# Performance work log

Measured on AMD Instinct MI355X. Metric: run time of the kernel, lower is better.

The kernel has to match this reference:

```python
import jax, jax.numpy as jnp
import numpy as np

A, H, DK, DM = 13, 16, 4, 256   # num_attention, n_head, d_k, d_model
DH = DM // H                    # per-head value dim = 16
MLP_OUT = 128
EPS = 1e-5
TEMP = float(np.sqrt(DK))
IN_CH = 10


def setup_inputs() -> dict:
    key = jax.random.key(0)
    ks = jax.random.split(key, 12)
    B, T = 1024, 60
    x = jax.random.normal(ks[0], (B, T, IN_CH), dtype=jnp.float32)
    # inconv (1x1 Conv1d == Linear over channels)
    Wc = jax.random.normal(ks[1], (DM, IN_CH), dtype=jnp.float32) * 0.1
    bc = jax.random.normal(ks[2], (DM,), dtype=jnp.float32) * 0.01
    # in_norm GroupNorm affine
    gn_in_w = jnp.ones((DM,), jnp.float32)
    gn_in_b = jnp.zeros((DM,), jnp.float32)
    # learned query + key projection (std = sqrt(2/d_k) per torch init)
    Q = jax.random.normal(ks[3], (A, H, DK), dtype=jnp.float32) * float(np.sqrt(2.0 / DK))
    Wk = jax.random.normal(ks[4], (A * H * DK, DM), dtype=jnp.float32) * float(np.sqrt(2.0 / DK))
    bk = jnp.zeros((A * H * DK,), jnp.float32)
    # MLP: Linear(256,128) + BatchNorm1d(128) (eval mode) + ReLU
    W1 = jax.random.normal(ks[5], (MLP_OUT, DM), dtype=jnp.float32) * 0.05
    b1 = jnp.zeros((MLP_OUT,), jnp.float32)
    bn_w = jnp.ones((MLP_OUT,), jnp.float32)
    bn_b = jnp.zeros((MLP_OUT,), jnp.float32)
    bn_rm = jnp.zeros((MLP_OUT,), jnp.float32)
    bn_rv = jnp.ones((MLP_OUT,), jnp.float32)
    # out_norm GroupNorm affine
    gn_out_w = jnp.ones((MLP_OUT,), jnp.float32)
    gn_out_b = jnp.zeros((MLP_OUT,), jnp.float32)
    return dict(x=x, Wc=Wc, bc=bc, gn_in_w=gn_in_w, gn_in_b=gn_in_b, Q=Q,
                Wk=Wk, bk=bk, W1=W1, b1=b1, bn_w=bn_w, bn_b=bn_b,
                bn_rm=bn_rm, bn_rv=bn_rv, gn_out_w=gn_out_w, gn_out_b=gn_out_b)


def _ltae_fwd(x, Wc, bc, gn_in_w, gn_in_b, Q, Wk, bk, W1, b1,
              bn_w, bn_b, bn_rm, bn_rv, gn_out_w, gn_out_b):
    B, T, _ = x.shape
    # inconv: 1x1 conv over channel dim
    h = jnp.einsum('btc,dc->btd', x, Wc) + bc                      # [B,T,DM]
    # in_norm: GroupNorm(H groups) over [B, DM, T] -> normalize per (sample, group) over (C/G, T)
    g = h.transpose(0, 2, 1).reshape(B, H, DM // H, T)
    mu = g.mean(axis=(2, 3), keepdims=True)
    var = g.var(axis=(2, 3), keepdims=True)
    g = (g - mu) / jnp.sqrt(var + EPS)
    v = (g.reshape(B, DM, T) * gn_in_w[None, :, None] + gn_in_b[None, :, None]).transpose(0, 2, 1)
    # ---- MultiHeadAttention (faithful to original reshape/view ordering) ----
    # q: stack Q along batch dim 2 then flatten -> row order (a, h, b)
    q = jnp.broadcast_to(Q[:, :, None, :], (A, H, B, DK)).reshape(-1, DK)      # [A*H*B, DK]
    # k: Linear then permute(3,0,1,2,4).view(-1,T,DK) (reproduces torch's contiguous flatten)
    k = (jnp.einsum('btd,ed->bte', v, Wk) + bk).reshape(B, T, A, H, DK)
    k = k.transpose(3, 0, 1, 2, 4).reshape(-1, T, DK)                          # [H*B*A, T, DK]
    # v heads: stack(split) -> [H, B, T, DH] -> [H*B, T, DH]
    vh = v.reshape(B, T, H, DH).transpose(2, 0, 1, 3).reshape(H * B, T, DH)
    attn = jnp.einsum('nd,ntd->nt', q, k) / TEMP                               # [N, T]
    attn = jax.nn.softmax(attn, axis=-1)                                       # dropout = identity (eval)
    ve = jnp.broadcast_to(vh[:, None], (H * B, A, T, DH)).reshape(-1, T, DH)   # [H*B*A, T, DH]
    out = jnp.einsum('nt,ntd->nd', attn, ve)                                   # [N, DH]
    out = out.reshape(A, H, B, DH)
    # ---- head concat + MLP ----
    out = out.transpose(0, 2, 1, 3).reshape(A * B, DM)
    y = out @ W1.T + b1
    y = (y - bn_rm) / jnp.sqrt(bn_rv + EPS) * bn_w + bn_b                      # BatchNorm1d eval
    y = jax.nn.relu(y)                                                          # dropout = identity (eval)
    # out_norm: GroupNorm(H, MLP_OUT) on 2D input: per-sample per-group norm
    g = y.reshape(A * B, H, MLP_OUT // H)
    mu = g.mean(axis=2, keepdims=True)
    var = g.var(axis=2, keepdims=True)
    y = ((g - mu) / jnp.sqrt(var + EPS)).reshape(A * B, MLP_OUT) * gn_out_w + gn_out_b
    return y.reshape(A, B, MLP_OUT).transpose(1, 0, 2)                          # [B, A, MLP_OUT]


def reference(x, Wc, bc, gn_in_w, gn_in_b, Q, Wk, bk, W1, b1,
              bn_w, bn_b, bn_rm, bn_rv, gn_out_w, gn_out_b):
    return _ltae_fwd(x, Wc, bc, gn_in_w, gn_in_b, Q, Wk, bk, W1, b1,
                     bn_w, bn_b, bn_rm, bn_rv, gn_out_w, gn_out_b)
```

## Files before the change

kernel.cpp:

```cpp
#include <hip/hip_runtime.h>
#include <hip/hip_bf16.h>
#include <math.h>

#define NB   1024
#define NT   60
#define NC   10
#define NDM  256
#define NH   16
#define NDH  16
#define NA   13
#define NM   208
#define NMO  128

#define WROW6 4096

#define OFF_WEFF  0
#define N_WEFF    (NH*14*WROW6)
#define OFF_BEFF  (OFF_WEFF + N_WEFF)
#define N_BEFF    (NM*NH*NA)
#define OFF_VGT   (OFF_BEFF + N_BEFF)
#define N_VGT     (NB*NDM*64)
#define OFF_ATT   (OFF_VGT + N_VGT)
#define N_ATT     (NM*NB*NDH)

#define LDS_FENCE() __asm__ __volatile__("s_waitcnt lgkmcnt(0)" ::: "memory")

__global__ void ltae_weff(const float* __restrict__ Q, const float* __restrict__ Wk,
                          const float* __restrict__ bk, float* __restrict__ weff6,
                          float* __restrict__ beff2) {
    int blk = blockIdx.x;
    int hk = blk / 14, mi = blk - hk*14;
    int m  = hk*13 + mi;
    int mc = m > 207 ? 207 : m;
    int d = threadIdx.x;
    float q0 = Q[mc*4+0], q1 = Q[mc*4+1], q2 = Q[mc*4+2], q3 = Q[mc*4+3];
    int g = d >> 1, dl = d & 1;
    size_t base = (size_t)blk*WROW6 + g*32 + dl*13;
#pragma unroll
    for (int ak = 0; ak < NA; ++ak) {
        int e = (ak*16 + hk)*4;
        float w = q0*Wk[(size_t)(e+0)*NDM + d] + q1*Wk[(size_t)(e+1)*NDM + d]
                + q2*Wk[(size_t)(e+2)*NDM + d] + q3*Wk[(size_t)(e+3)*NDM + d];
        weff6[base + ak] = w;
    }
    if (dl == 1) {
#pragma unroll
        for (int p = 26; p < 32; ++p) weff6[(size_t)blk*WROW6 + g*32 + p] = 0.f;
    }
    if (d < NA && m <= 207) {
        int e = (d*16 + hk)*4;
        beff2[(m*16 + hk)*NA + d] = q0*bk[e] + q1*bk[e+1] + q2*bk[e+2] + q3*bk[e+3];
    }
}

#define VT_S 66
#define K1_LDS_BYTES ((NDM*VT_S + NT*NC)*4)

__launch_bounds__(1024, 8)
__global__ void ltae_convgn(const float* __restrict__ x, const float* __restrict__ Wc,
                            const float* __restrict__ bc, const float* __restrict__ gnw,
                            const float* __restrict__ gnb, float* __restrict__ vgT) {
    extern __shared__ float smem[];
    float* Vt = smem;
    float* xs = smem + NDM*VT_S;
    int b = blockIdx.x, tid = threadIdx.x;
    if (tid < NT*NC) xs[tid] = x[(size_t)b*NT*NC + tid];
    __syncthreads();
    {
        int d = tid >> 2, q = tid & 3;
        float wc[NC];
#pragma unroll
        for (int c = 0; c < NC; ++c) wc[c] = Wc[d*NC + c];
        float bcv = bc[d];
        float h[15];
        float s1 = 0.f, s2 = 0.f;
#pragma unroll
        for (int k = 0; k < 15; ++k) {
            int t = 15*q + k;
            float a = bcv;
#pragma unroll
            for (int c = 0; c < NC; ++c) a = fmaf(xs[t*NC + c], wc[c], a);
            h[k] = a; s1 += a; s2 += a*a;
        }
#pragma unroll
        for (int off = 1; off < 64; off <<= 1) {
            s1 += __shfl_xor(s1, off);
            s2 += __shfl_xor(s2, off);
        }
        float mean = s1 * (1.f/960.f);
        float var  = s2 * (1.f/960.f) - mean*mean;
        float rstd = rsqrtf(var + 1e-5f);
        float g = gnw[d], bb = gnb[d];
#pragma unroll
        for (int k = 0; k < 15; ++k)
            Vt[d*VT_S + 15*q + k] = (h[k]-mean)*rstd*g + bb;
    }
    __syncthreads();
    float* vb = vgT + (size_t)b*NDM*64;
    for (int i = tid; i < NDM*16; i += 1024) {
        int d = i >> 4, t4 = (i & 15) << 2;
        float4 o;
        o.x = (t4+0 < NT) ? Vt[d*VT_S + t4+0] : 0.f;
        o.y = (t4+1 < NT) ? Vt[d*VT_S + t4+1] : 0.f;
        o.z = (t4+2 < NT) ? Vt[d*VT_S + t4+2] : 0.f;
        o.w = (t4+3 < NT) ? Vt[d*VT_S + t4+3] : 0.f;
        *(float4*)&vb[d*64 + t4] = o;
    }
}

#define BSTRIDE (NDM*64)
__launch_bounds__(128, 8)
__global__ void ltae_attn(const float* __restrict__ vgT, const float* __restrict__ weff6,
                          const float* __restrict__ beff2, float* __restrict__ attout) {
    __shared__ float wbuf[2*784];
    int p = blockIdx.x;
    int xcd = p & 7, idx = p >> 3;
    int b   = xcd * 128 + (idx >> 3);
    int hkp = idx & 7;
    int tid = threadIdx.x;
    int wid = tid >> 6, lane = tid & 63;
    int hk = __builtin_amdgcn_readfirstlane(hkp*2 + wid);
    int tk = lane;
    int mi0   = (13*b) >> 10;
    int rstar = ((mi0+1) << 10) - 13*b;
    const float* __restrict__ wrow = weff6 + (size_t)(hk*14 + mi0)*WROW6;
    const float* __restrict__ vX   = vgT + (size_t)b*BSTRIDE + tk;
    float* myC = wbuf + wid*784;

    float acc[13];
#pragma unroll
    for (int j = 0; j < 13; ++j) acc[j] = 0.f;

#pragma unroll 1
    for (int gg = 0; gg < 64; ++gg) {
        const float* wgA = wrow + (size_t)(2*gg)*32;
        const float* wgB = wrow + (size_t)(2*gg+1)*32;
        float a0 = vX[(4*gg+0)*64];
        float a1 = vX[(4*gg+1)*64];
        float c0 = vX[(4*gg+2)*64];
        float c1 = vX[(4*gg+3)*64];
#pragma unroll
        for (int ak = 0; ak < 13; ++ak)
            acc[ak] = fmaf(a1, wgA[13+ak], fmaf(a0, wgA[ak], acc[ak]));
#pragma unroll
        for (int ak = 0; ak < 13; ++ak)
            acc[ak] = fmaf(c1, wgB[13+ak], fmaf(c0, wgB[ak], acc[ak]));
    }

    if (rstar < 13) {
        int ustar = 60*rstar;
        int tstar = (ustar >= 1) ? (ustar/13) : -1;
        if (tk == tstar) {
#pragma unroll
            for (int j = 0; j < 13; ++j) myC[j] = acc[j];
        }
        LDS_FENCE();
        if (tk >= tstar) {
#pragma unroll
            for (int j = 0; j < 13; ++j) acc[j] = 0.f;
            const float* __restrict__ wrow2 = weff6 + (size_t)(hk*14 + mi0 + 1)*WROW6;
#pragma unroll 1
            for (int g = 0; g < 128; ++g) {
                const float* wg = wrow2 + g*32;
                float v0 = vX[(2*g)*64];
                float v1 = vX[(2*g+1)*64];
#pragma unroll
                for (int ak = 0; ak < 13; ++ak)
                    acc[ak] = fmaf(v1, wg[13+ak], fmaf(v0, wg[ak], acc[ak]));
            }
        }
        if (tk == tstar) {
#pragma unroll
            for (int j = 0; j < 13; ++j)
                if (13*tk + j < ustar) acc[j] = myC[j];
        }
        LDS_FENCE();
    }

    int dh = lane >> 2, cc = lane & 3;
    int hb13 = (hk*1024 + b)*13;
    if (tk < NT) {
#pragma unroll
        for (int j = 0; j < 13; ++j) myC[13*tk + j] = acc[j];
    }
    LDS_FENCE();
    float vreg[15];
#pragma unroll
    for (int j = 0; j < 15; ++j)
        vreg[j] = vgT[((size_t)b*NDM + hk*16 + dh)*64 + cc + 4*j];
#pragma unroll 1
    for (int r = 0; r < 13; ++r) {
        int n = hb13 + r;
        int m = n >> 10;
        int brow = (m*16 + hk)*13;
        float logit = -1e30f;
        if (lane < NT) {
            int u  = r*60 + lane;
            int ak = u % 13;
            logit = (myC[u] + beff2[brow + ak]) * 0.5f;
        }
        float mx = logit;
#pragma unroll
        for (int off = 32; off; off >>= 1) mx = fmaxf(mx, __shfl_xor(mx, off));
        float e = (lane < NT) ? __expf(logit - mx) : 0.f;
        float s = e;
#pragma unroll
        for (int off = 32; off; off >>= 1) s += __shfl_xor(s, off);
        float attn = e / s;
        if (lane < NT) myC[r*60 + lane] = attn;
        LDS_FENCE();
        float a = 0.f;
#pragma unroll
        for (int j = 0; j < 15; ++j)
            a = fmaf(myC[r*60 + cc + 4*j], vreg[j], a);
        a += __shfl_xor(a, 1);
        a += __shfl_xor(a, 2);
        if (cc == 0) attout[(size_t)n*NDH + dh] = a;
    }
}

#define FS 260
__launch_bounds__(1024)
__global__ void ltae_mlp(const float* __restrict__ attout, const float* __restrict__ W1,
                         const float* __restrict__ b1, const float* __restrict__ bnw,
                         const float* __restrict__ bnb, const float* __restrict__ bnrm,
                         const float* __restrict__ bnrv, const float* __restrict__ gow,
                         const float* __restrict__ gob, float* __restrict__ out) {
    __shared__ float f[16*FS];
    int tid = threadIdx.x;
    int sl  = tid & 7;
    int j   = tid >> 3;
    int base = blockIdx.x << 4;
    for (int k = tid; k < 16*NDM; k += 1024) {
        int s = k >> 8, c = k & 255;
        int sid2 = base + s;
        int aa = sid2 >> 10, bb = sid2 & 1023;
        int h2 = c >> 4, dhh = c & 15;
        f[s*FS + c] = attout[((size_t)((aa*16 + h2)*1024 + bb))*NDH + dhh];
    }
    __syncthreads();
    const float* fr0 = f + sl*FS;
    const float* fr1 = f + (sl+8)*FS;
    const float* w   = &W1[(size_t)j*NDM];
    float bj = b1[j];
    float acc0 = bj, acc1 = bj;
    for (int c = 0; c < NDM; c += 4) {
        float4 wv = *(const float4*)&w[c];
        float4 f0 = *(const float4*)&fr0[c];
        float4 f1 = *(const float4*)&fr1[c];
        acc0 += wv.x*f0.x + wv.y*f0.y + wv.z*f0.z + wv.w*f0.w;
        acc1 += wv.x*f1.x + wv.y*f1.y + wv.z*f1.z + wv.w*f1.w;
    }
    float rs = rsqrtf(bnrv[j] + 1e-5f);
    float sc = rs * bnw[j];
    float sh = bnb[j] - bnrm[j]*sc;
    float y0 = fmaxf(acc0*sc + sh, 0.f);
    float y1 = fmaxf(acc1*sc + sh, 0.f);
    float a1 = y0, b1s = y0*y0, a2 = y1, b2s = y1*y1;
#pragma unroll
    for (int off = 8; off < 64; off <<= 1) {
        a1  += __shfl_xor(a1, off);
        b1s += __shfl_xor(b1s, off);
        a2  += __shfl_xor(a2, off);
        b2s += __shfl_xor(b2s, off);
    }
    float gw = gow[j], gb = gob[j];
    {
        float mean = a1 * 0.125f;
        float var  = b1s * 0.125f - mean*mean;
        float o = (y0 - mean) * rsqrtf(var + 1e-5f) * gw + gb;
        int sid = base + sl, aa = sid >> 10, bb = sid & 1023;
        out[((size_t)bb*NA + aa)*NMO + j] = o;
    }
    {
        float mean = a2 * 0.125f;
        float var  = b2s * 0.125f - mean*mean;
        float o = (y1 - mean) * rsqrtf(var + 1e-5f) * gw + gb;
        int sid = base + sl + 8, aa = sid >> 10, bb = sid & 1023;
        out[((size_t)bb*NA + aa)*NMO + j] = o;
    }
}

extern "C" void kernel_launch(void* const* d_in, const int* in_sizes, int n_in,
                              void* d_out, int out_size, void* d_ws, size_t ws_size,
                              hipStream_t stream) {
    const float* x    = (const float*)d_in[0];
    const float* Wc   = (const float*)d_in[1];
    const float* bc   = (const float*)d_in[2];
    const float* gnw  = (const float*)d_in[3];
    const float* gnb  = (const float*)d_in[4];
    const float* Q    = (const float*)d_in[5];
    const float* Wk   = (const float*)d_in[6];
    const float* bk   = (const float*)d_in[7];
    const float* W1   = (const float*)d_in[8];
    const float* b1   = (const float*)d_in[9];
    const float* bnw  = (const float*)d_in[10];
    const float* bnb  = (const float*)d_in[11];
    const float* bnrm = (const float*)d_in[12];
    const float* bnrv = (const float*)d_in[13];
    const float* gow  = (const float*)d_in[14];
    const float* gob  = (const float*)d_in[15];

    float* ws     = (float*)d_ws;
    float* weff6  = ws + OFF_WEFF;
    float* beff2  = ws + OFF_BEFF;
    float* vgT    = ws + OFF_VGT;
    float* attout = ws + OFF_ATT;
    float* outp   = (float*)d_out;

    hipLaunchKernelGGL(ltae_weff, dim3(NH*14), dim3(256), 0, stream, Q, Wk, bk, weff6, beff2);
    hipFuncSetAttribute((const void*)ltae_convgn,
                        hipFuncAttributeMaxDynamicSharedMemorySize, K1_LDS_BYTES);
    hipLaunchKernelGGL(ltae_convgn, dim3(NB), dim3(1024), K1_LDS_BYTES, stream,
                       x, Wc, bc, gnw, gnb, vgT);
    hipLaunchKernelGGL(ltae_attn, dim3(8192), dim3(128), 0, stream,
                       vgT, weff6, beff2, attout);
    hipLaunchKernelGGL(ltae_mlp, dim3(NA*NB/16), dim3(1024), 0, stream,
                       attout, W1, b1, bnw, bnb, bnrm, bnrv, gow, gob, outp);
}
```

Measured before the change: 292.7 us.

## Store normalized values time-major so attention loads become vector loads

Result: slower. 328.4 us (+12.2%).

```diff
diff --git a/kernel.cpp b/kernel.cpp
--- a/kernel.cpp
+++ b/kernel.cpp
@@ -13,6 +13,8 @@
 #define NMO  128
 
 #define WROW6 4096
+
+#define BSTRIDE (NDM*64)
 
 #define OFF_WEFF  0
 #define N_WEFF    (NH*14*WROW6)
@@ -96,19 +98,22 @@
             Vt[d*VT_S + 15*q + k] = (h[k]-mean)*rstd*g + bb;
     }
     __syncthreads();
-    float* vb = vgT + (size_t)b*NDM*64;
-    for (int i = tid; i < NDM*16; i += 1024) {
-        int d = i >> 4, t4 = (i & 15) << 2;
+    float* vb = vgT + (size_t)b*BSTRIDE;
+    for (int i = tid; i < 64*64; i += 1024) {
+        int t = i >> 6, q = i & 63;
         float4 o;
-        o.x = (t4+0 < NT) ? Vt[d*VT_S + t4+0] : 0.f;
-        o.y = (t4+1 < NT) ? Vt[d*VT_S + t4+1] : 0.f;
-        o.z = (t4+2 < NT) ? Vt[d*VT_S + t4+2] : 0.f;
-        o.w = (t4+3 < NT) ? Vt[d*VT_S + t4+3] : 0.f;
-        *(float4*)&vb[d*64 + t4] = o;
-    }
-}
-
-#define BSTRIDE (NDM*64)
+        if (t < NT) {
+            o.x = Vt[(4*q+0)*VT_S + t];
+            o.y = Vt[(4*q+1)*VT_S + t];
+            o.z = Vt[(4*q+2)*VT_S + t];
+            o.w = Vt[(4*q+3)*VT_S + t];
+        } else {
+            o.x = o.y = o.z = o.w = 0.f;
+        }
+        *(float4*)&vb[t*NDM + 4*q] = o;
+    }
+}
+
 __launch_bounds__(128, 8)
 __global__ void ltae_attn(const float* __restrict__ vgT, const float* __restrict__ weff6,
                           const float* __restrict__ beff2, float* __restrict__ attout) {
@@ -124,7 +129,7 @@
     int mi0   = (13*b) >> 10;
     int rstar = ((mi0+1) << 10) - 13*b;
     const float* __restrict__ wrow = weff6 + (size_t)(hk*14 + mi0)*WROW6;
-    const float* __restrict__ vX   = vgT + (size_t)b*BSTRIDE + tk;
+    const float* __restrict__ vX   = vgT + (size_t)b*BSTRIDE + (size_t)tk*NDM;
     float* myC = wbuf + wid*784;
 
     float acc[13];
@@ -132,19 +137,25 @@
     for (int j = 0; j < 13; ++j) acc[j] = 0.f;
 
 #pragma unroll 1
-    for (int gg = 0; gg < 64; ++gg) {
-        const float* wgA = wrow + (size_t)(2*gg)*32;
-        const float* wgB = wrow + (size_t)(2*gg+1)*32;
-        float a0 = vX[(4*gg+0)*64];
-        float a1 = vX[(4*gg+1)*64];
-        float c0 = vX[(4*gg+2)*64];
-        float c1 = vX[(4*gg+3)*64];
+    for (int gg = 0; gg < 32; ++gg) {
+        const float* wg0 = wrow + (size_t)(4*gg)*32;
+        const float* wg1 = wg0 + 32;
+        const float* wg2 = wg0 + 64;
+        const float* wg3 = wg0 + 96;
+        float4 A = *(const float4*)&vX[8*gg];
+        float4 B = *(const float4*)&vX[8*gg + 4];
 #pragma unroll
         for (int ak = 0; ak < 13; ++ak)
-            acc[ak] = fmaf(a1, wgA[13+ak], fmaf(a0, wgA[ak], acc[ak]));
+            acc[ak] = fmaf(A.y, wg0[13+ak], fmaf(A.x, wg0[ak], acc[ak]));
 #pragma unroll
         for (int ak = 0; ak < 13; ++ak)
-            acc[ak] = fmaf(c1, wgB[13+ak], fmaf(c0, wgB[ak], acc[ak]));
+            acc[ak] = fmaf(A.w, wg1[13+ak], fmaf(A.z, wg1[ak], acc[ak]));
+#pragma unroll
+        for (int ak = 0; ak < 13; ++ak)
+            acc[ak] = fmaf(B.y, wg2[13+ak], fmaf(B.x, wg2[ak], acc[ak]));
+#pragma unroll
+        for (int ak = 0; ak < 13; ++ak)
+            acc[ak] = fmaf(B.w, wg3[13+ak], fmaf(B.z, wg3[ak], acc[ak]));
     }
 
     if (rstar < 13) {
@@ -162,11 +173,10 @@
 #pragma unroll 1
             for (int g = 0; g < 128; ++g) {
                 const float* wg = wrow2 + g*32;
-                float v0 = vX[(2*g)*64];
-                float v1 = vX[(2*g+1)*64];
+                float2 v01 = *(const float2*)&vX[2*g];
 #pragma unroll
                 for (int ak = 0; ak < 13; ++ak)
-                    acc[ak] = fmaf(v1, wg[13+ak], fmaf(v0, wg[ak], acc[ak]));
+                    acc[ak] = fmaf(v01.y, wg[13+ak], fmaf(v01.x, wg[ak], acc[ak]));
             }
         }
         if (tk == tstar) {
@@ -187,7 +197,7 @@
     float vreg[15];
 #pragma unroll
     for (int j = 0; j < 15; ++j)
-        vreg[j] = vgT[((size_t)b*NDM + hk*16 + dh)*64 + cc + 4*j];
+        vreg[j] = vgT[(size_t)b*BSTRIDE + (size_t)(cc + 4*j)*NDM + hk*16 + dh];
 #pragma unroll 1
     for (int r = 0; r < 13; ++r) {
         int n = hb13 + r;
```
